# Performance work log

Measured on AMD Instinct MI355X. Metric: run time of the kernel, lower is better.

The kernel has to match this reference:

```python
import jax, jax.numpy as jnp
import numpy as np

N_NODES = 100000
N_EDGES = 3200000
N_FEAT = 16
N_LAYERS = 4


def setup_inputs() -> dict:
    key = jax.random.key(0)
    k1, k2, k3, k4 = jax.random.split(key, 4)
    h_0 = jax.random.normal(k1, (N_NODES, N_FEAT), dtype=jnp.float32)
    edge_index = jax.random.randint(k2, (2, N_EDGES), 0, N_NODES, dtype=jnp.int64)
    weight_tensor = jax.random.normal(k3, (N_EDGES,), dtype=jnp.float32)
    # per-layer learned per-edge weights, init normal(std=1/sqrt(E)) as in torch
    layer_weights = jax.random.normal(k4, (N_LAYERS, N_EDGES), dtype=jnp.float32) / np.sqrt(N_EDGES)
    return {"h_0": h_0, "edge_index": edge_index, "weight_tensor": weight_tensor,
            "layer_weights": layer_weights}


def _layer(h, src, dst, edge_scale):
    # gather x_j = h[src]  [E, F], scale by per-edge scalar, scatter-add to dst
    msg = edge_scale[:, None] * h[src]
    return jax.ops.segment_sum(msg, dst, num_segments=N_NODES)


def reference(h_0, edge_index, weight_tensor, layer_weights):
    # PyG default flow source_to_target: x_j = x[edge_index[0]], aggregate at edge_index[1]
    src = edge_index[0]
    dst = edge_index[1]
    h = h_0
    for k in range(N_LAYERS - 1):
        h = _layer(h, src, dst, weight_tensor * layer_weights[k])
        h = h + h_0
    h = _layer(h, src, dst, weight_tensor * layer_weights[N_LAYERS - 1])
    return jax.nn.sigmoid(2.0 * h)
```

## Files before the change

kernel.cpp:

```cpp
#include <hip/hip_runtime.h>
#include <hip/hip_fp16.h>

#define NNODES   100000
#define NFEAT    16
#define NEDGES   3200000
#define EH       1600000
#define NB       250
#define NODES_PB 400
#define NCHH     500
#define NCH2     1000
#define CHK      3200
#define CAP      7168
#define N8       (NNODES * 8)

__global__ __launch_bounds__(256) void hist_chunk(
    const int* __restrict__ dst, int* __restrict__ cnt )
{
    __shared__ int h[NB];
    int c = blockIdx.x;
    for (int i = threadIdx.x; i < NB; i += 256) h[i] = 0;
    __syncthreads();
    int base = c * CHK;
    for (int i = threadIdx.x; i < CHK; i += 256) {
        int d = dst[base + i];
        atomicAdd(&h[d / NODES_PB], 1);
    }
    __syncthreads();
    for (int i = threadIdx.x; i < NB; i += 256) cnt[c * NB + i] = h[i];
}

__global__ __launch_bounds__(512) void scan_chunks(
    int* __restrict__ cnt, int* __restrict__ tot )
{
    __shared__ int x[512];
    int half = blockIdx.x / NB;
    int b    = blockIdx.x % NB;
    int t = threadIdx.x;
    int v = (t < NCHH) ? cnt[(half * NCHH + t) * NB + b] : 0;
    x[t] = v;
    __syncthreads();
    for (int off = 1; off < 512; off <<= 1) {
        int y = (t >= off) ? x[t - off] : 0;
        __syncthreads();
        x[t] += y;
        __syncthreads();
    }
    if (t < NCHH) cnt[(half * NCHH + t) * NB + b] = x[t] - v;
    if (t == NCHH - 1) tot[half * NB + b] = x[t];
}

__global__ __launch_bounds__(256) void scan_tot(
    const int* __restrict__ tot, int* __restrict__ bb)
{
    __shared__ int x[256];
    int half = blockIdx.x;
    const int* tt = tot + half * NB;
    int* bbh = bb + half * (NB + 1);
    int t = threadIdx.x;
    int v = (t < NB) ? tt[t] : 0;
    x[t] = v;
    __syncthreads();
    for (int off = 1; off < 256; off <<= 1) {
        int y = (t >= off) ? x[t - off] : 0;
        __syncthreads();
        x[t] += y;
        __syncthreads();
    }
    if (t < NB) bbh[t] = x[t] - v;
    if (t == NB - 1) bbh[NB] = x[t];
}

__global__ __launch_bounds__(512) void scatter_bins(
    const int*   __restrict__ src,
    const int*   __restrict__ dst,
    const float* __restrict__ wt,
    const float* __restrict__ lw,
    const int*   __restrict__ cnt,
    const int*   __restrict__ tot,
    const int*   __restrict__ bb,
    unsigned int* __restrict__ binsE )
{
    __shared__ unsigned int   sE[CHK * 3];
    __shared__ unsigned short sB[CHK];
    __shared__ int lhist[NB];
    __shared__ int loff[NB];
    __shared__ int lcur[NB];
    __shared__ int gmb[NB];
    __shared__ int x[512];

    int c = blockIdx.x;
    int t = threadIdx.x;
    int half = c / NCHH;
    int cc   = c % NCHH;
    const int* bbh = bb + half * (NB + 1);
    unsigned int* bE = binsE + (size_t)half * 3 * EH;

    for (int i = t; i < NB; i += 512) {
        int cur0 = cnt[c * NB + i];
        int nxt  = (cc == NCHH - 1) ? tot[half * NB + i] : cnt[(c + 1) * NB + i];
        lhist[i] = nxt - cur0;
        gmb[i]   = bbh[i] + cur0;
    }
    __syncthreads();
    int v = (t < NB) ? lhist[t] : 0;
    x[t] = v;
    __syncthreads();
    for (int off = 1; off < 512; off <<= 1) {
        int y = (t >= off) ? x[t - off] : 0;
        __syncthreads();
        x[t] += y;
        __syncthreads();
    }
    if (t < NB) {
        int excl = x[t] - v;
        loff[t] = excl;
        lcur[t] = excl;
        gmb[t] -= excl;
    }
    __syncthreads();

    int base = c * CHK;
    for (int i = t; i < CHK; i += 512) {
        int e = base + i;
        int d = dst[e];
        int b  = d / NODES_PB;
        int dl = d - b * NODES_PB;
        float w = wt[e];
        __half2 w01 = __floats2half2_rn(w * lw[e],              w * lw[NEDGES + e]);
        __half2 w23 = __floats2half2_rn(w * lw[2 * NEDGES + e], w * lw[3 * NEDGES + e]);
        int slot = atomicAdd(&lcur[b], 1);
        sE[3 * slot + 0] = (unsigned int)src[e] | ((unsigned int)dl << 17);
        sE[3 * slot + 1] = *(const unsigned int*)&w01;
        sE[3 * slot + 2] = *(const unsigned int*)&w23;
        sB[slot] = (unsigned short)b;
    }
    __syncthreads();

    for (int s = t; s < CHK; s += 512) {
        int b = sB[s];
        unsigned int g = (unsigned int)(gmb[b] + s);
        unsigned int* p = bE + 3u * g;
        p[0] = sE[3 * s + 0];
        p[1] = sE[3 * s + 1];
        p[2] = sE[3 * s + 2];
    }
}

__global__ __launch_bounds__(512) void bucket_csr(
    const int*          __restrict__ bb,
    const unsigned int* __restrict__ binsE,
    unsigned int*       __restrict__ csrA   ,
    unsigned short*     __restrict__ wbase  ,
    int*                __restrict__ offs   )
{
    __shared__ unsigned int   regA[CAP];
    __shared__ unsigned int   regC[CAP];
    __shared__ unsigned short pi[CAP];
    __shared__ int hist[NODES_PB];
    __shared__ int cur[NODES_PB];
    __shared__ int sc[512];
    int g = blockIdx.x, t = threadIdx.x;
    int half = g / NB;
    int b    = g % NB;
    const int* bbh = bb + half * (NB + 1);
    const unsigned int* bE = binsE + (size_t)half * 3 * EH;
    unsigned int*   cA = csrA + (size_t)half * EH;
    unsigned short* w0 = wbase + (size_t)(half * 4 + 0) * EH;
    unsigned short* w1 = wbase + (size_t)(half * 4 + 1) * EH;
    unsigned short* w2 = wbase + (size_t)(half * 4 + 2) * EH;
    unsigned short* w3 = wbase + (size_t)(half * 4 + 3) * EH;
    int* offsh = offs + half * (NNODES + 1);

    int e0 = bbh[b];
    int cnt = bbh[b + 1] - e0;
    if (cnt > CAP) cnt = CAP;

    for (int i = t; i < NODES_PB; i += 512) hist[i] = 0;
    __syncthreads();
    for (int i = t; i < cnt; i += 512) {
        unsigned int a = bE[3u * (unsigned int)(e0 + i)];
        regA[i] = a;
        atomicAdd(&hist[a >> 17], 1);
    }
    __syncthreads();
    int v = (t < NODES_PB) ? hist[t] : 0;
    sc[t] = v;
    __syncthreads();
    for (int off = 1; off < 512; off <<= 1) {
        int y = (t >= off) ? sc[t - off] : 0;
        __syncthreads();
        sc[t] += y;
        __syncthreads();
    }
    if (t < NODES_PB) {
        int excl = sc[t] - v;
        cur[t] = excl;
        offsh[b * NODES_PB + t] = e0 + excl;
    }
    if (b == 0 && t == 0) offsh[NNODES] = EH;
    __syncthreads();
    unsigned short* inv = (unsigned short*)regC;
    for (int i = t; i < cnt; i += 512) {
        unsigned int a = regA[i];
        int slot = atomicAdd(&cur[a >> 17], 1);
        pi[i]  = (unsigned short)slot;
        inv[slot] = (unsigned short)i;
    }
    __syncthreads();
    for (int s = t; s < cnt; s += 512) {
        cA[e0 + s] = regA[inv[s]] & 0x1FFFFu;
    }
    __syncthreads();
    unsigned short* wA0 = (unsigned short*)regA;
    unsigned short* wA1 = wA0 + CAP;
    unsigned short* wC2 = (unsigned short*)regC;
    unsigned short* wC3 = wC2 + CAP;
    for (int i = t; i < cnt; i += 512) {
        unsigned int u01 = bE[3u * (unsigned int)(e0 + i) + 1];
        unsigned int u23 = bE[3u * (unsigned int)(e0 + i) + 2];
        int s = pi[i];
        wA0[s] = (unsigned short)(u01 & 0xFFFFu);
        wA1[s] = (unsigned short)(u01 >> 16);
        wC2[s] = (unsigned short)(u23 & 0xFFFFu);
        wC3[s] = (unsigned short)(u23 >> 16);
    }
    __syncthreads();
    for (int s = t; s < cnt; s += 512) {
        w0[e0 + s] = wA0[s];
        w1[e0 + s] = wA1[s];
        w2[e0 + s] = wC2[s];
        w3[e0 + s] = wC3[s];
    }
}

__global__ __launch_bounds__(256) void conv16(
    const float2* __restrict__ in, __half2* __restrict__ out, int n2)
{
    int i = blockIdx.x * 256 + threadIdx.x;
    if (i < n2) {
        float2 v = in[i];
        out[i] = __floats2half2_rn(v.x, v.y);
    }
}

template<bool SIG>
__global__ __launch_bounds__(256) void pullr(
    const int*            __restrict__ offs1,
    const int*            __restrict__ offs2,
    const unsigned int*   __restrict__ csrA1,
    const unsigned int*   __restrict__ csrA2,
    const unsigned short* __restrict__ wk1,
    const unsigned short* __restrict__ wk2,
    const __half2*        __restrict__ h16,
    const float2*         __restrict__ h0,
    void*                 __restrict__ hout)
{
    int t = blockIdx.x * 256 + threadIdx.x;
    int n = t >> 5;
    if (n >= NNODES) return;
    int grp = (t >> 3) & 3;
    int f2  = t & 7;

    int j01 = offs1[n], e1 = offs1[n + 1];
    int j02 = offs2[n], e2 = offs2[n + 1];
    int m1 = (j01 + e1) >> 1;
    int m2 = (j02 + e2) >> 1;

    const unsigned int*   A;
    const unsigned short* W;
    int js, je;
    if (grp < 2) {
        A = csrA1; W = wk1;
        js = (grp == 0) ? j01 : m1;
        je = (grp == 0) ? m1  : e1;
    } else {
        A = csrA2; W = wk2;
        js = (grp == 2) ? j02 : m2;
        je = (grp == 2) ? m2  : e2;
    }

    float ax = 0.f, ay = 0.f;
    int j = js;
    for (; j + 3 < je; j += 4) {
        unsigned int s0 = A[j],     s1 = A[j + 1];
        unsigned int s2 = A[j + 2], s3 = A[j + 3];
        float w0 = __half2float(__ushort_as_half(W[j]));
        float w1 = __half2float(__ushort_as_half(W[j + 1]));
        float w2 = __half2float(__ushort_as_half(W[j + 2]));
        float w3 = __half2float(__ushort_as_half(W[j + 3]));
        float2 v0 = __half22float2(h16[s0 * 8 + f2]);
        float2 v1 = __half22float2(h16[s1 * 8 + f2]);
        float2 v2 = __half22float2(h16[s2 * 8 + f2]);
        float2 v3 = __half22float2(h16[s3 * 8 + f2]);
        ax = fmaf(w0, v0.x, ax); ay = fmaf(w0, v0.y, ay);
        ax = fmaf(w1, v1.x, ax); ay = fmaf(w1, v1.y, ay);
        ax = fmaf(w2, v2.x, ax); ay = fmaf(w2, v2.y, ay);
        ax = fmaf(w3, v3.x, ax); ay = fmaf(w3, v3.y, ay);
    }
    for (; j < je; ++j) {
        unsigned int s = A[j];
        float w = __half2float(__ushort_as_half(W[j]));
        float2 v = __half22float2(h16[s * 8 + f2]);
        ax = fmaf(w, v.x, ax); ay = fmaf(w, v.y, ay);
    }

    ax += __shfl_xor(ax, 8);  ay += __shfl_xor(ay, 8);
    ax += __shfl_xor(ax, 16); ay += __shfl_xor(ay, 16);

    if (grp == 0) {
        int o = n * 8 + f2;
        if (SIG) {
            float2 r;
            r.x = 1.f / (1.f + expf(-2.f * ax));
            r.y = 1.f / (1.f + expf(-2.f * ay));
            ((float2*)hout)[o] = r;
        } else {
            float2 b = h0[o];
            ((__half2*)hout)[o] = __floats2half2_rn(ax + b.x, ay + b.y);
        }
    }
}

__global__ __launch_bounds__(256) void scatter_layer(
    const int* __restrict__ src, const int* __restrict__ dst,
    const float* __restrict__ wt, const float* __restrict__ lw,
    const float* __restrict__ h, float* __restrict__ acc)
{
    long t = (long)blockIdx.x * blockDim.x + threadIdx.x;
    int e = (int)(t >> 4);
    if (e >= NEDGES) return;
    int f = (int)(t & 15);
    float w = wt[e] * lw[e];
    atomicAdd(&acc[dst[e] * NFEAT + f], w * h[src[e] * NFEAT + f]);
}
__global__ __launch_bounds__(256) void sigmoid_inplace(float* __restrict__ out, int n)
{
    int i = blockIdx.x * blockDim.x + threadIdx.x;
    if (i < n) out[i] = 1.f / (1.f + expf(-2.f * out[i]));
}

extern "C" void kernel_launch(void* const* d_in, const int* in_sizes, int n_in,
                              void* d_out, int out_size, void* d_ws, size_t ws_size,
                              hipStream_t stream)
{
    const float* h0 = (const float*)d_in[0];
    const int*   ei = (const int*)d_in[1];
    const float* wt = (const float*)d_in[2];
    const float* lw = (const float*)d_in[3];

    const int* src = ei;
    const int* dst = ei + NEDGES;

    const size_t off_cnt  = 0;
    const size_t off_tot  = 1000064;
    const size_t off_bb   = 1002112;
    const size_t off_offs = 1004160;
    const size_t off_csrA = 1804288;
    const size_t off_w    = off_csrA + (size_t)2 * EH * 4;
    const size_t off_bins = off_w + (size_t)8 * EH * 2;
    const size_t need     = off_bins + (size_t)2 * 3 * EH * 4;

    if (ws_size < need) {
        const size_t hbytes = (size_t)NNODES * NFEAT * sizeof(float);
        float* hw = (float*)d_ws;
        float* ho = (float*)d_out;
        dim3 blk(256), grd(((long)NEDGES * 16 + 255) / 256);
        hipMemcpyAsync(hw, h0, hbytes, hipMemcpyDeviceToDevice, stream);
        scatter_layer<<<grd, blk, 0, stream>>>(src, dst, wt, lw + 0L * NEDGES, h0, hw);
        hipMemcpyAsync(ho, h0, hbytes, hipMemcpyDeviceToDevice, stream);
        scatter_layer<<<grd, blk, 0, stream>>>(src, dst, wt, lw + 1L * NEDGES, hw, ho);
        hipMemcpyAsync(hw, h0, hbytes, hipMemcpyDeviceToDevice, stream);
        scatter_layer<<<grd, blk, 0, stream>>>(src, dst, wt, lw + 2L * NEDGES, ho, hw);
        hipMemsetAsync(ho, 0, hbytes, stream);
        scatter_layer<<<grd, blk, 0, stream>>>(src, dst, wt, lw + 3L * NEDGES, hw, ho);
        int n = NNODES * NFEAT;
        sigmoid_inplace<<<(n + 255) / 256, 256, 0, stream>>>(ho, n);
        return;
    }

    char* ws = (char*)d_ws;
    int*            cnt   = (int*)(ws + off_cnt);
    int*            tot   = (int*)(ws + off_tot);
    int*            bb    = (int*)(ws + off_bb);
    int*            offs  = (int*)(ws + off_offs);
    int*            offs1 = offs;
    int*            offs2 = offs + (NNODES + 1);
    unsigned int*   csrA  = (unsigned int*)(ws + off_csrA);
    unsigned int*   csrA1 = csrA;
    unsigned int*   csrA2 = csrA + EH;
    unsigned short* wbase = (unsigned short*)(ws + off_w);
    unsigned short* w0_1 = wbase + 0L * EH; unsigned short* w1_1 = wbase + 1L * EH;
    unsigned short* w2_1 = wbase + 2L * EH; unsigned short* w3_1 = wbase + 3L * EH;
    unsigned short* w0_2 = wbase + 4L * EH; unsigned short* w1_2 = wbase + 5L * EH;
    unsigned short* w2_2 = wbase + 6L * EH; unsigned short* w3_2 = wbase + 7L * EH;
    unsigned int*   binsE = (unsigned int*)(ws + off_bins);
    const size_t HB = (size_t)NNODES * NFEAT * 2;
    __half2* hb0  = (__half2*)(ws + off_bins);
    __half2* hbA  = (__half2*)(ws + off_bins + HB);
    __half2* hbB  = (__half2*)d_out;
    float*   hout = (float*)d_out;

    hist_chunk  <<<NCH2,   256, 0, stream>>>(dst, cnt);
    scan_chunks <<<2 * NB, 512, 0, stream>>>(cnt, tot);
    scan_tot    <<<2,      256, 0, stream>>>(tot, bb);
    scatter_bins<<<NCH2,   512, 0, stream>>>(src, dst, wt, lw, cnt, tot, bb, binsE);
    bucket_csr  <<<2 * NB, 512, 0, stream>>>(bb, binsE, csrA, wbase, offs);

    conv16<<<(N8 + 255) / 256, 256, 0, stream>>>((const float2*)h0, hb0, N8);

    dim3 blk(256), grdP((NNODES * 32) / 256);
    const float2* h0f2 = (const float2*)h0;
    pullr<false><<<grdP, blk, 0, stream>>>(offs1, offs2, csrA1, csrA2, w0_1, w0_2, hb0, h0f2, hbA);
    pullr<false><<<grdP, blk, 0, stream>>>(offs1, offs2, csrA1, csrA2, w1_1, w1_2, hbA, h0f2, hbB);
    pullr<false><<<grdP, blk, 0, stream>>>(offs1, offs2, csrA1, csrA2, w2_1, w2_2, hbB, h0f2, hbA);
    pullr<true ><<<grdP, blk, 0, stream>>>(offs1, offs2, csrA1, csrA2, w3_1, w3_2, hbA, h0f2, hout);
}
```

Measured before the change: 207.8 us.

## Widen pull kernel to 64 lanes per node and flatten bin copy-out

```diff
diff --git a/kernel.cpp b/kernel.cpp
--- a/kernel.cpp
+++ b/kernel.cpp
@@ -82,8 +82,6 @@
 {
     __shared__ unsigned int   sE[CHK * 3];
     __shared__ unsigned short sB[CHK];
-    __shared__ int lhist[NB];
-    __shared__ int loff[NB];
     __shared__ int lcur[NB];
     __shared__ int gmb[NB];
     __shared__ int x[512];
@@ -95,15 +93,14 @@
     const int* bbh = bb + half * (NB + 1);
     unsigned int* bE = binsE + (size_t)half * 3 * EH;
 
-    for (int i = t; i < NB; i += 512) {
-        int cur0 = cnt[c * NB + i];
-        int nxt  = (cc == NCHH - 1) ? tot[half * NB + i] : cnt[(c + 1) * NB + i];
-        lhist[i] = nxt - cur0;
-        gmb[i]   = bbh[i] + cur0;
-    }
-    __syncthreads();
-    int v = (t < NB) ? lhist[t] : 0;
-    x[t] = v;
+    int myLen = 0, myBase = 0;
+    if (t < NB) {
+        int cur0 = cnt[c * NB + t];
+        int nxt  = (cc == NCHH - 1) ? tot[half * NB + t] : cnt[(c + 1) * NB + t];
+        myLen  = nxt - cur0;
+        myBase = bbh[t] + cur0;
+    }
+    x[t] = myLen;
     __syncthreads();
     for (int off = 1; off < 512; off <<= 1) {
         int y = (t >= off) ? x[t - off] : 0;
@@ -112,10 +109,9 @@
         __syncthreads();
     }
     if (t < NB) {
-        int excl = x[t] - v;
-        loff[t] = excl;
+        int excl = x[t] - myLen;
         lcur[t] = excl;
-        gmb[t] -= excl;
+        gmb[t]  = 3 * (myBase - excl);
     }
     __syncthreads();
 
@@ -136,13 +132,10 @@
     }
     __syncthreads();
 
-    for (int s = t; s < CHK; s += 512) {
+    for (int idx = t; idx < 3 * CHK; idx += 512) {
+        int s = (idx * 21846) >> 16;
         int b = sB[s];
-        unsigned int g = (unsigned int)(gmb[b] + s);
-        unsigned int* p = bE + 3u * g;
-        p[0] = sE[3 * s + 0];
-        p[1] = sE[3 * s + 1];
-        p[2] = sE[3 * s + 2];
+        bE[gmb[b] + idx] = sE[idx];
     }
 }
 
@@ -256,28 +249,22 @@
     void*                 __restrict__ hout)
 {
     int t = blockIdx.x * 256 + threadIdx.x;
-    int n = t >> 5;
+    int n = t >> 6;
     if (n >= NNODES) return;
-    int grp = (t >> 3) & 3;
+    int grp = (t >> 3) & 7;
     int f2  = t & 7;
-
-    int j01 = offs1[n], e1 = offs1[n + 1];
-    int j02 = offs2[n], e2 = offs2[n + 1];
-    int m1 = (j01 + e1) >> 1;
-    int m2 = (j02 + e2) >> 1;
 
     const unsigned int*   A;
     const unsigned short* W;
-    int js, je;
-    if (grp < 2) {
-        A = csrA1; W = wk1;
-        js = (grp == 0) ? j01 : m1;
-        je = (grp == 0) ? m1  : e1;
+    int j0, len;
+    if (grp < 4) {
+        j0 = offs1[n]; len = offs1[n + 1] - j0; A = csrA1; W = wk1;
     } else {
-        A = csrA2; W = wk2;
-        js = (grp == 2) ? j02 : m2;
-        je = (grp == 2) ? m2  : e2;
-    }
+        j0 = offs2[n]; len = offs2[n + 1] - j0; A = csrA2; W = wk2;
+    }
+    int q  = grp & 3;
+    int js = j0 + ((len * q) >> 2);
+    int je = j0 + ((len * (q + 1)) >> 2);
 
     float ax = 0.f, ay = 0.f;
     int j = js;
@@ -306,6 +293,7 @@
 
     ax += __shfl_xor(ax, 8);  ay += __shfl_xor(ay, 8);
     ax += __shfl_xor(ax, 16); ay += __shfl_xor(ay, 16);
+    ax += __shfl_xor(ax, 32); ay += __shfl_xor(ay, 32);
 
     if (grp == 0) {
         int o = n * 8 + f2;
@@ -408,7 +396,7 @@
 
     conv16<<<(N8 + 255) / 256, 256, 0, stream>>>((const float2*)h0, hb0, N8);
 
-    dim3 blk(256), grdP((NNODES * 32) / 256);
+    dim3 blk(256), grdP((NNODES * 64) / 256);
     const float2* h0f2 = (const float2*)h0;
     pullr<false><<<grdP, blk, 0, stream>>>(offs1, offs2, csrA1, csrA2, w0_1, w0_2, hb0, h0f2, hbA);
     pullr<false><<<grdP, blk, 0, stream>>>(offs1, offs2, csrA1, csrA2, w1_1, w1_2, hbA, h0f2, hbB);
```

Result: slower. 255.6 us (+23.0%).
